# Kernel optimization log

Measured on AMD Instinct MI355X. Metric: run time of the kernel, lower is better.

Reference implementation:

```python
import jax, jax.numpy as jnp
import numpy as np

N_E = 1024
E_DIM = 256
BETA = 0.25
N = 131072


def setup_inputs() -> dict:
    key = jax.random.key(0)
    k1, k2 = jax.random.split(key)
    z = jax.random.normal(k1, (N, E_DIM), dtype=jnp.float32)
    # original init: uniform(-1/n_e, 1/n_e)
    emb_weight = jax.random.uniform(k2, (N_E, E_DIM), dtype=jnp.float32,
                                    minval=-1.0 / N_E, maxval=1.0 / N_E)
    return {"z": z, "emb_weight": emb_weight}


def reference(z, emb_weight):
    # pairwise squared distances: ||z||^2 + ||e||^2 - 2 z @ e^T   -> [N, n_e]
    d = (jnp.sum(z * z, axis=1, keepdims=True)
         + jnp.sum(emb_weight * emb_weight, axis=1)
         - 2.0 * jnp.matmul(z, emb_weight.T))
    min_encoding_indices = jnp.argmin(d, axis=1)            # [N]
    z_q = emb_weight[min_encoding_indices]                  # gather == one-hot matmul
    sg = jax.lax.stop_gradient
    loss = (jnp.mean((sg(z_q) - z) ** 2)
            + BETA * jnp.mean((z_q - sg(z)) ** 2))
    z_q_st = z + sg(z_q - z)                                # straight-through
    return z_q_st, loss, min_encoding_indices[:, None]
```

## Files before the change

### kernel.cpp

```cpp
#include <hip/hip_runtime.h>
#include <cfloat>

#define NROWS 131072
#define EDIM 256
#define NE 1024
#define DELTA 2.0e-4f

#define BM 128
#define BN 128
#define BK 32

typedef unsigned short u16;
typedef __attribute__((ext_vector_type(8))) short bf16x8;
typedef __attribute__((ext_vector_type(4))) float f32x4;

#define WS_Z2    0u
#define WS_E2    524288u
#define WS_PART  528384u
#define WS_CNT   548864u
#define WS_LIST  549120u
#define WS_CI1   1073408u
#define WS_CI2   1597696u
#define WS_FLG   2121984u
#define WS_BP    2646272u
#define WS_END   4219136u

__device__ __forceinline__ float np_sumsq256(const float* __restrict__ row) {
    float s[2];
#pragma unroll
    for (int h = 0; h < 2; ++h) {
        const float* a = row + h * 128;
        float r[8];
#pragma unroll
        for (int j = 0; j < 8; ++j) r[j] = __fmul_rn(a[j], a[j]);
        for (int i = 8; i < 128; i += 8) {
#pragma unroll
            for (int j = 0; j < 8; ++j)
                r[j] = __fadd_rn(r[j], __fmul_rn(a[i + j], a[i + j]));
        }
        s[h] = __fadd_rn(__fadd_rn(__fadd_rn(r[0], r[1]), __fadd_rn(r[2], r[3])),
                         __fadd_rn(__fadd_rn(r[4], r[5]), __fadd_rn(r[6], r[7])));
    }
    return __fadd_rn(s[0], s[1]);
}

__device__ __forceinline__ u16 bf16_rn(float x) {
    unsigned u = __float_as_uint(x);
    return (u16)((u + 0x7fffu + ((u >> 16) & 1u)) >> 16);
}

__global__ __launch_bounds__(256)
void rownorm_split_kernel(const float* __restrict__ z, float* __restrict__ z2out,
                          u16* __restrict__ zhi, u16* __restrict__ zlo) {
    __shared__ float zl[16 * 256];
    const int tid = threadIdx.x;
    const size_t base4 = (size_t)blockIdx.x * 1024;

    {
        const float4* src = reinterpret_cast<const float4*>(z) + base4;
        float4* dst = reinterpret_cast<float4*>(zl);
#pragma unroll
        for (int i = 0; i < 4; ++i) dst[tid + 256 * i] = src[tid + 256 * i];
    }
    __syncthreads();

    {
        const int row = tid >> 4;
        const int j16 = tid & 15;
        const int h = j16 >> 3, j = j16 & 7;
        const float* a = &zl[row * 256 + h * 128];
        float r = __fmul_rn(a[j], a[j]);
#pragma unroll
        for (int i = 8; i < 128; i += 8)
            r = __fadd_rn(r, __fmul_rn(a[i + j], a[i + j]));
        r = __fadd_rn(r, __shfl_xor(r, 1));
        r = __fadd_rn(r, __shfl_xor(r, 2));
        r = __fadd_rn(r, __shfl_xor(r, 4));
        r = __fadd_rn(r, __shfl_xor(r, 8));
        if (j16 == 0) z2out[blockIdx.x * 16 + row] = r;
    }

    {
        ushort4* ph = reinterpret_cast<ushort4*>(zhi) + base4;
        ushort4* pl = reinterpret_cast<ushort4*>(zlo) + base4;
        const float4* sp = reinterpret_cast<const float4*>(zl);
#pragma unroll
        for (int i = 0; i < 4; ++i) {
            const int q = tid + 256 * i;
            float4 v = sp[q];
            float xs[4] = {v.x, v.y, v.z, v.w};
            u16 hh[4], lo[4];
#pragma unroll
            for (int c = 0; c < 4; ++c) {
                u16 hv = bf16_rn(xs[c]);
                float hf = __uint_as_float(((unsigned)hv) << 16);
                hh[c] = hv;
                lo[c] = bf16_rn(__fsub_rn(xs[c], hf));
            }
            ph[q] = make_ushort4(hh[0], hh[1], hh[2], hh[3]);
            pl[q] = make_ushort4(lo[0], lo[1], lo[2], lo[3]);
        }
    }
}

__global__ __launch_bounds__(256)
void rownorm_kernel(const float* __restrict__ x, float* __restrict__ out, int nrows) {
    int row = blockIdx.x * blockDim.x + threadIdx.x;
    if (row < nrows) out[row] = np_sumsq256(x + (size_t)row * EDIM);
}

__global__ __launch_bounds__(256)
void build_b_kernel(const float* __restrict__ e, u16* __restrict__ Bp) {
    int idx = blockIdx.x * 256 + threadIdx.x;
    int row = idx >> 8, k = idx & 255;
    float x = e[idx];
    u16 hh = bf16_rn(x);
    float hf = __uint_as_float(((unsigned)hh) << 16);
    u16 lo = bf16_rn(__fsub_rn(x, hf));
    Bp[row * 512 + k] = hh;
    Bp[row * 512 + 256 + k] = lo;
}

__device__ __forceinline__ void gload_lds16(const void* g, void* lds) {
    __builtin_amdgcn_global_load_lds((const __attribute__((address_space(1))) void*)g,
                                     (__attribute__((address_space(3))) void*)lds,
                                     16, 0, 0);
}

#define LEXLT(va, ia, vb, ib) ((va) < (vb) || ((va) == (vb) && (ia) < (ib)))

#define MERGE5(a1, ai1, a2, ai2, a3, b1, bi1, b2, bi2, b3)                    \
    {                                                                         \
        float n1v, n2v, n3v; int n1i, n2i;                                    \
        if (LEXLT(a1, ai1, b1, bi1)) {                                        \
            n1v = a1; n1i = ai1;                                              \
            if (LEXLT(a2, ai2, b1, bi1)) { n2v = a2; n2i = ai2; n3v = fminf(a3, b1); } \
            else                          { n2v = b1; n2i = bi1; n3v = fminf(a2, b2); } \
        } else {                                                              \
            n1v = b1; n1i = bi1;                                              \
            if (LEXLT(b2, bi2, a1, ai1)) { n2v = b2; n2i = bi2; n3v = fminf(b3, a1); } \
            else                          { n2v = a1; n2i = ai1; n3v = fminf(b2, a2); } \
        }                                                                     \
        a1 = n1v; ai1 = n1i; a2 = n2v; ai2 = n2i; a3 = n3v;                   \
    }

__global__ __launch_bounds__(512, 2)
void vq_mfma_kernel(const u16* __restrict__ zhi, const u16* __restrict__ zlo,
                    const u16* __restrict__ Bp, const float* __restrict__ e2f,
                    int* __restrict__ ci1, int* __restrict__ ci2, int* __restrict__ cflag) {
    __shared__ __align__(16) u16  At[128 * 64];
    __shared__ __align__(16) u16  Bt[256 * 64];
    __shared__ float e2s[1024];
    __shared__ float mrg[128 * 4 * 4];

    const int tid = threadIdx.x;
    const int m0  = blockIdx.x * 128;
    const int l   = tid & 63;
    const int wid = tid >> 6;
    const int wrg = wid >> 2;
    const int wcg = wid & 3;
    const int lr  = l & 15;
    const int lg  = l >> 4;
    const int key = lr & 7;

    e2s[tid] = e2f[tid];
    e2s[tid + 512] = e2f[tid + 512];

    const int rsub = tid >> 3;
    const int lch  = (tid & 7) ^ (rsub & 7);

#define STAGE_AT(src, colc)                                                   \
    {                                                                         \
        _Pragma("unroll")                                                     \
        for (int s = 0; s < 2; ++s)                                           \
            gload_lds16((src) + (size_t)(m0 + s * 64 + rsub) * 256 + (colc) + lch * 8, \
                        At + (size_t)(s * 512 + tid) * 8);                    \
    }
#define STAGE_BT(off)                                                         \
    {                                                                         \
        _Pragma("unroll")                                                     \
        for (int s = 0; s < 4; ++s)                                           \
            gload_lds16(Bp + (size_t)(n0 + s * 64 + rsub) * 512 + (off) + lch * 8, \
                        Bt + (size_t)(s * 512 + tid) * 8);                    \
    }
#define MFMA_STEP()                                                           \
    {                                                                         \
        const u16* Ebase = Bt + (wcg * 64 + lr) * 64;                         \
        const u16* Zbase = At + (wrg * 64 + lr) * 64;                         \
        _Pragma("unroll")                                                     \
        for (int kk = 0; kk < 2; ++kk) {                                      \
            const int go = ((kk * 4 + lg) ^ key) * 8;                         \
            bf16x8 a[4], b[4];                                                \
            _Pragma("unroll")                                                 \
            for (int fr = 0; fr < 4; ++fr)                                    \
                a[fr] = *reinterpret_cast<const bf16x8*>(Ebase + fr * 1024 + go); \
            _Pragma("unroll")                                                 \
            for (int fc = 0; fc < 4; ++fc)                                    \
                b[fc] = *reinterpret_cast<const bf16x8*>(Zbase + fc * 1024 + go); \
            _Pragma("unroll")                                                 \
            for (int fr = 0; fr < 4; ++fr)                                    \
                _Pragma("unroll")                                             \
                for (int fc = 0; fc < 4; ++fc)                                \
                    acc[fr][fc] = __builtin_amdgcn_mfma_f32_16x16x32_bf16(    \
                        a[fr], b[fc], acc[fr][fc], 0, 0, 0);                  \
        }                                                                     \
    }

    float v1[4], v2[4], v3[4];
    unsigned pidx[4];
#pragma unroll
    for (int s = 0; s < 4; ++s) { v1[s] = FLT_MAX; v2[s] = FLT_MAX; v3[s] = FLT_MAX; pidx[s] = 0; }

#pragma unroll 1
    for (int nc = 0; nc < 4; ++nc) {
        const int n0 = nc * 256;
        f32x4 acc[4][4];
#pragma unroll
        for (int fr = 0; fr < 4; ++fr)
#pragma unroll
            for (int fc = 0; fc < 4; ++fc) acc[fr][fc] = (f32x4){0.f, 0.f, 0.f, 0.f};

#pragma unroll 1
        for (int j = 0; j < 4; ++j) {
            __syncthreads();
            STAGE_AT(zhi, j * 64);
            STAGE_BT(j * 64);
            asm volatile("s_waitcnt vmcnt(0)" ::: "memory");
            __syncthreads();
            MFMA_STEP();

            __syncthreads();
            STAGE_BT(256 + j * 64);
            asm volatile("s_waitcnt vmcnt(0)" ::: "memory");
            __syncthreads();
            MFMA_STEP();
        }
#pragma unroll 1
        for (int j = 0; j < 4; ++j) {
            __syncthreads();
            STAGE_AT(zlo, j * 64);
            STAGE_BT(j * 64);
            asm volatile("s_waitcnt vmcnt(0)" ::: "memory");
            __syncthreads();
            MFMA_STEP();
        }

#pragma unroll
        for (int fr = 0; fr < 4; ++fr) {
            const int cbase = n0 + wcg * 64 + fr * 16 + lg * 4;
            const float4 e2v = *reinterpret_cast<const float4*>(&e2s[cbase]);
#pragma unroll
            for (int q = 0; q < 4; ++q) {
                const unsigned n = (unsigned)(cbase + q);
                const float e2q = (q == 0) ? e2v.x : (q == 1) ? e2v.y : (q == 2) ? e2v.z : e2v.w;
#pragma unroll
                for (int fc = 0; fc < 4; ++fc) {
                    float d = __fmaf_rn(-2.0f, acc[fr][fc][q], e2q);
                    bool lt1 = d < v1[fc];
                    bool lt2 = d < v2[fc];
                    bool lt3 = d < v3[fc];
                    v3[fc] = lt2 ? v2[fc] : (lt3 ? d : v3[fc]);
                    v2[fc] = lt1 ? v1[fc] : (lt2 ? d : v2[fc]);
                    pidx[fc] = lt1 ? ((pidx[fc] << 16) | n)
                                   : (lt2 ? ((pidx[fc] & 0xffffu) | (n << 16)) : pidx[fc]);
                    v1[fc] = lt1 ? d : v1[fc];
                }
            }
        }
    }

#pragma unroll
    for (int s = 0; s < 4; ++s) {
        float a1 = v1[s], a2 = v2[s], a3 = v3[s];
        int ai1 = (int)(pidx[s] & 0xffffu), ai2 = (int)(pidx[s] >> 16);
#pragma unroll
        for (int m = 16; m <= 32; m <<= 1) {
            float b1 = __shfl_xor(a1, m), b2 = __shfl_xor(a2, m), b3 = __shfl_xor(a3, m);
            int bi1 = __shfl_xor(ai1, m), bi2 = __shfl_xor(ai2, m);
            MERGE5(a1, ai1, a2, ai2, a3, b1, bi1, b2, bi2, b3);
        }
        if (lg == 0) {
            int row = wrg * 64 + s * 16 + lr;
            float* p = &mrg[(row * 4 + wcg) * 4];
            p[0] = a1; p[1] = a2; p[2] = a3;
            p[3] = __uint_as_float(((unsigned)ai1 & 0xffffu) | ((unsigned)ai2 << 16));
        }
    }
    __syncthreads();

    if (tid < 128) {
        const float* p0 = &mrg[(tid * 4 + 0) * 4];
        float A1 = p0[0], A2 = p0[1], A3 = p0[2];
        unsigned pk = __float_as_uint(p0[3]);
        int I1 = (int)(pk & 0xffffu), I2 = (int)(pk >> 16);
#pragma unroll
        for (int w = 1; w < 4; ++w) {
            const float* p = &mrg[(tid * 4 + w) * 4];
            float b1 = p[0], b2 = p[1], b3 = p[2];
            unsigned q = __float_as_uint(p[3]);
            int bi1 = (int)(q & 0xffffu), bi2 = (int)(q >> 16);
            MERGE5(A1, I1, A2, I2, A3, b1, bi1, b2, bi2, b3);
        }
        ci1[m0 + tid] = I1;
        ci2[m0 + tid] = I2;
        cflag[m0 + tid] = (A3 - A1 <= DELTA) ? 1 : 0;
    }
}

__device__ __forceinline__ float exact_g(const float* __restrict__ zr,
                                         const float* __restrict__ er,
                                         float z2v, float e2v) {
    float m = 0.f;
    for (int k = 0; k < 256; k += 4) {
        float4 zv = *reinterpret_cast<const float4*>(zr + k);
        float4 ev = *reinterpret_cast<const float4*>(er + k);
        m = __fmaf_rn(zv.x, ev.x, m);
        m = __fmaf_rn(zv.y, ev.y, m);
        m = __fmaf_rn(zv.z, ev.z, m);
        m = __fmaf_rn(zv.w, ev.w, m);
    }
    return __fsub_rn(__fadd_rn(z2v, e2v), __fmul_rn(2.0f, m));
}

__global__ __launch_bounds__(256)
void vq_refine_kernel(const float* __restrict__ z, const float* __restrict__ e,
                      const float* __restrict__ z2g, const float* __restrict__ e2f,
                      const int* __restrict__ ci1, const int* __restrict__ ci2,
                      const int* __restrict__ cflag,
                      float* __restrict__ out_idx, int* __restrict__ list,
                      int* __restrict__ counter,
                      float* __restrict__ out_zq, double* __restrict__ partials) {
    __shared__ float  gbuf[128];
    __shared__ int    fIdx[64];
    __shared__ int    fFlag[64];
    __shared__ double dred[256];
    const int tid = threadIdx.x;
    const int r0  = blockIdx.x * 64;

    if (tid < 128) {
        int r = tid >> 1, which = tid & 1;
        int row = r0 + r;
        int c = which ? ci2[row] : ci1[row];
        gbuf[tid] = exact_g(z + (size_t)row * EDIM, e + (size_t)c * EDIM, z2g[row], e2f[c]);
    }
    __syncthreads();
    if (tid < 64) {
        int row = r0 + tid;
        int a = ci1[row], b = ci2[row];
        float ga = gbuf[tid * 2], gb = gbuf[tid * 2 + 1];
        int fi = (gb < ga || (gb == ga && b < a)) ? b : a;
        fIdx[tid] = fi;
        int fl = cflag[row];
        fFlag[tid] = fl;
        out_idx[row] = (float)fi;
        if (fl) { int p = atomicAdd(counter, 1); list[p] = row; }
    }
    __syncthreads();

    double lsum = 0.0;
    for (int r = 0; r < 64; ++r) {
        if (!fFlag[r]) {
            int row = r0 + r;
            float zv = z[(size_t)row * EDIM + tid];
            float ev = e[(size_t)fIdx[r] * EDIM + tid];
            float dd = __fsub_rn(ev, zv);
            out_zq[(size_t)row * EDIM + tid] = __fadd_rn(zv, dd);
            lsum += (double)dd * (double)dd;
        }
    }
    dred[tid] = lsum;
    __syncthreads();
#pragma unroll
    for (int s = 128; s > 0; s >>= 1) {
        if (tid < s) dred[tid] += dred[tid + s];
        __syncthreads();
    }
    if (tid == 0) partials[blockIdx.x] = dred[0];
}

__global__ __launch_bounds__(256)
void vq_fallback_kernel(const float* __restrict__ z, const float* __restrict__ e,
                        const float* __restrict__ z2g, const float* __restrict__ e2f,
                        const int* __restrict__ list, const int* __restrict__ counter,
                        float* __restrict__ out_idx, float* __restrict__ out_zq,
                        double* __restrict__ partials2) {
    __shared__ float  elds[64 * 257];
    __shared__ float  zlds[4][256];
    __shared__ float  z2s[4];
    __shared__ double dred[256];
    const int n   = *counter;
    const int tid = threadIdx.x;
    const int w   = tid >> 6;
    const int lane = tid & 63;
    double lsum = 0.0;

    for (int base = blockIdx.x * 4; base < n; base += gridDim.x * 4) {
        const int nr = min(4, n - base);
        __syncthreads();
        for (int i = tid; i < nr * 256; i += 256)
            zlds[i >> 8][i & 255] = z[(size_t)list[base + (i >> 8)] * EDIM + (i & 255)];
        if (tid < nr) z2s[tid] = z2g[list[base + tid]];

        float bv = FLT_MAX; int bi = 0x7fffffff;
        const int srow  = ((tid >> 4) & 3);
        const int scolq = (tid & 15) | ((tid >> 6) << 4);
        for (int c0 = 0; c0 < NE; c0 += 64) {
            __syncthreads();
#pragma unroll
            for (int s = 0; s < 16; ++s) {
                int row = 4 * s + srow;
                float4 v = *reinterpret_cast<const float4*>(e + (size_t)(c0 + row) * EDIM + scolq * 4);
                float* d = &elds[row * 257 + scolq * 4];
                d[0] = v.x; d[1] = v.y; d[2] = v.z; d[3] = v.w;
            }
            __syncthreads();
            const int code = c0 + lane;
            const float* er = &elds[lane * 257];
            const float* zr = zlds[w];
            float m = 0.f;
#pragma unroll 8
            for (int k = 0; k < 256; ++k)
                m = __fmaf_rn(zr[k], er[k], m);
            float g = __fsub_rn(__fadd_rn(z2s[w], e2f[code]), __fmul_rn(2.0f, m));
            if (g < bv || (g == bv && code < bi)) { bv = g; bi = code; }
        }
#pragma unroll
        for (int m2 = 1; m2 < 64; m2 <<= 1) {
            float ov = __shfl_xor(bv, m2); int oi = __shfl_xor(bi, m2);
            if (ov < bv || (ov == bv && oi < bi)) { bv = ov; bi = oi; }
        }
        if (w < nr) {
            int row = list[base + w];
            if (lane == 0) out_idx[row] = (float)bi;
            const float* er2 = e + (size_t)bi * EDIM;
            for (int c = lane; c < 256; c += 64) {
                float zv = zlds[w][c];
                float dd = __fsub_rn(er2[c], zv);
                out_zq[(size_t)row * EDIM + c] = __fadd_rn(zv, dd);
                lsum += (double)dd * (double)dd;
            }
        }
    }
    dred[tid] = lsum;
    __syncthreads();
#pragma unroll
    for (int s = 128; s > 0; s >>= 1) {
        if (tid < s) dred[tid] += dred[tid + s];
        __syncthreads();
    }
    if (tid == 0) partials2[blockIdx.x] = dred[0];
}

__global__ void vq_loss_kernel(const double* __restrict__ partials, int count,
                               float* __restrict__ out_loss) {
    __shared__ double s[256];
    const int tid = threadIdx.x;
    double v = 0.0;
    for (int i = tid; i < count; i += 256) v += partials[i];
    s[tid] = v;
    __syncthreads();
    for (int k = 128; k > 0; k >>= 1) {
        if (tid < k) s[tid] += s[tid + k];
        __syncthreads();
    }
    if (tid == 0) {
        double mean = s[0] / ((double)NROWS * (double)EDIM);
        out_loss[0] = (float)(1.25 * mean);
    }
}

__global__ __launch_bounds__(256, 2)
void vq_main_r3(const float* __restrict__ z, const float* __restrict__ e,
                const float* __restrict__ z2g, const float* __restrict__ e2g,
                float* __restrict__ out_zq, float* __restrict__ out_idx,
                double* __restrict__ partials) {
    __shared__ float A[BK][BM];
    __shared__ float Bm[BK][BN];
    __shared__ float e2s[BN];
    __shared__ int   fIdx[BM];
    __shared__ double dred[256];
    const int tid = threadIdx.x;
    const int m0 = blockIdx.x * BM;
    const int trow = tid >> 4, tcol = tid & 15;
    float z2r[8];
#pragma unroll
    for (int i = 0; i < 8; ++i) z2r[i] = z2g[m0 + trow * 8 + i];
    float bestV[8]; int bestI[8];
#pragma unroll
    for (int i = 0; i < 8; ++i) { bestV[i] = FLT_MAX; bestI[i] = 0; }
    for (int n0 = 0; n0 < NE; n0 += BN) {
        float acc[8][8];
#pragma unroll
        for (int i = 0; i < 8; ++i)
#pragma unroll
            for (int j = 0; j < 8; ++j) acc[i][j] = 0.f;
        __syncthreads();
        if (tid < BN) e2s[tid] = e2g[n0 + tid];
        for (int k0 = 0; k0 < EDIM; k0 += BK) {
            __syncthreads();
#pragma unroll
            for (int s = 0; s < 4; ++s) {
                int q = tid + 256 * s, row = q >> 3, kc = (q & 7) << 2;
                float4 va = *reinterpret_cast<const float4*>(z + (size_t)(m0 + row) * EDIM + k0 + kc);
                A[kc + 0][row] = va.x; A[kc + 1][row] = va.y; A[kc + 2][row] = va.z; A[kc + 3][row] = va.w;
                float4 vb = *reinterpret_cast<const float4*>(e + (size_t)(n0 + row) * EDIM + k0 + kc);
                Bm[kc + 0][row] = vb.x; Bm[kc + 1][row] = vb.y; Bm[kc + 2][row] = vb.z; Bm[kc + 3][row] = vb.w;
            }
            __syncthreads();
#pragma unroll
            for (int k = 0; k < BK; ++k) {
                float a[8], b[8];
                *reinterpret_cast<float4*>(&a[0]) = *reinterpret_cast<const float4*>(&A[k][trow * 8]);
                *reinterpret_cast<float4*>(&a[4]) = *reinterpret_cast<const float4*>(&A[k][trow * 8 + 4]);
                *reinterpret_cast<float4*>(&b[0]) = *reinterpret_cast<const float4*>(&Bm[k][tcol * 8]);
                *reinterpret_cast<float4*>(&b[4]) = *reinterpret_cast<const float4*>(&Bm[k][tcol * 8 + 4]);
#pragma unroll
                for (int i = 0; i < 8; ++i)
#pragma unroll
                    for (int j = 0; j < 8; ++j) acc[i][j] = __fmaf_rn(a[i], b[j], acc[i][j]);
            }
        }
#pragma unroll
        for (int i = 0; i < 8; ++i)
#pragma unroll
            for (int j = 0; j < 8; ++j) {
                int n = n0 + tcol * 8 + j;
                float d = __fsub_rn(__fadd_rn(z2r[i], e2s[tcol * 8 + j]), __fmul_rn(2.0f, acc[i][j]));
                if (d < bestV[i]) { bestV[i] = d; bestI[i] = n; }
            }
    }
    __syncthreads();
    float* red_v = &A[0][0];
    int* red_i = reinterpret_cast<int*>(&Bm[0][0]);
#pragma unroll
    for (int i = 0; i < 8; ++i) {
        int row = trow * 8 + i;
        red_v[row * 16 + tcol] = bestV[i];
        red_i[row * 16 + tcol] = bestI[i];
    }
    __syncthreads();
    if (tid < BM) {
        float b1 = FLT_MAX; int i1 = 0x7fffffff;
        for (int t = 0; t < 16; ++t) {
            float v = red_v[tid * 16 + t]; int id = red_i[tid * 16 + t];
            if (v < b1 || (v == b1 && id < i1)) { b1 = v; i1 = id; }
        }
        fIdx[tid] = i1;
        out_idx[m0 + tid] = (float)i1;
    }
    __syncthreads();
    double lsum = 0.0;
    for (int r = 0; r < BM; ++r) {
        int fi = fIdx[r];
        float zv = z[(size_t)(m0 + r) * EDIM + tid];
        float ev = e[(size_t)fi * EDIM + tid];
        float dd = __fsub_rn(ev, zv);
        out_zq[(size_t)(m0 + r) * EDIM + tid] = __fadd_rn(zv, dd);
        lsum += (double)dd * (double)dd;
    }
    dred[tid] = lsum;
    __syncthreads();
#pragma unroll
    for (int s = 128; s > 0; s >>= 1) {
        if (tid < s) dred[tid] += dred[tid + s];
        __syncthreads();
    }
    if (tid == 0) partials[blockIdx.x] = dred[0];
}

extern "C" void kernel_launch(void* const* d_in, const int* in_sizes, int n_in,
                              void* d_out, int out_size, void* d_ws, size_t ws_size,
                              hipStream_t stream) {
    (void)n_in; (void)out_size;
    const float* z = (const float*)d_in[0];
    const float* e = (const float*)d_in[1];
    if (in_sizes[0] == NE * EDIM) { const float* t = z; z = e; e = t; }
    float* out      = (float*)d_out;
    float* out_zq   = out;
    float* out_loss = out + (size_t)NROWS * EDIM;
    float* out_idx  = out_loss + 1;

    char* ws = (char*)d_ws;
    float*  z2g      = (float*)(ws + WS_Z2);
    float*  e2f      = (float*)(ws + WS_E2);
    double* partials = (double*)(ws + WS_PART);

    rownorm_kernel<<<(NE + 255) / 256, 256, 0, stream>>>(e, e2f, NE);

    if (ws_size >= WS_END) {
        int* cnt  = (int*)(ws + WS_CNT);
        int* list = (int*)(ws + WS_LIST);
        int* ci1  = (int*)(ws + WS_CI1);
        int* ci2  = (int*)(ws + WS_CI2);
        int* flg  = (int*)(ws + WS_FLG);
        u16* Bp   = (u16*)(ws + WS_BP);
        u16* zhi  = (u16*)d_out;
        u16* zlo  = zhi + (size_t)NROWS * EDIM;

        hipMemsetAsync(cnt, 0, 4, stream);
        rownorm_split_kernel<<<NROWS / 16, 256, 0, stream>>>(z, z2g, zhi, zlo);
        build_b_kernel<<<NE * EDIM / 256, 256, 0, stream>>>(e, Bp);
        vq_mfma_kernel<<<NROWS / 128, 512, 0, stream>>>(zhi, zlo, Bp, e2f, ci1, ci2, flg);
        vq_refine_kernel<<<NROWS / 64, 256, 0, stream>>>(z, e, z2g, e2f, ci1, ci2, flg,
                                                         out_idx, list, cnt, out_zq, partials);
        vq_fallback_kernel<<<512, 256, 0, stream>>>(z, e, z2g, e2f, list, cnt,
                                                    out_idx, out_zq, partials + 2048);
        vq_loss_kernel<<<1, 256, 0, stream>>>(partials, 2560, out_loss);
    } else {
        rownorm_kernel<<<NROWS / 256, 256, 0, stream>>>(z, z2g, NROWS);
        vq_main_r3<<<NROWS / BM, 256, 0, stream>>>(z, e, z2g, e2f, out_zq, out_idx, partials);
        vq_loss_kernel<<<1, 256, 0, stream>>>(partials, 1024, out_loss);
    }
}
```

Baseline: 592.0 us.

## Double-buffer LDS tiles and enlarge MFMA block tile to 256 rows

Doubles the row tile per block from 128 to 256 and reorganizes waves as 4x2, with each wave computing an 8x4 fragment grid. It also double-buffers the A and B LDS tiles and unrolls the K schedule into explicit prefetch stages, using partial vmcnt waits so global-to-LDS loads overlap MFMA work. The goal is more data reuse per tile and hiding load latency instead of waiting for all loads before each step. In exchange, LDS use rises to about 128KB per block and the accumulators double, which can cut occupancy or force register spills under launch_bounds(512,2).

```diff
diff --git a/kernel.cpp b/kernel.cpp
--- a/kernel.cpp
+++ b/kernel.cpp
@@ -144,21 +144,24 @@
         a1 = n1v; ai1 = n1i; a2 = n2v; ai2 = n2i; a3 = n3v;                   \
     }
 
+#define WAITVM(N) asm volatile("s_waitcnt vmcnt(" #N ")" ::: "memory")
+#define RBAR()    asm volatile("s_barrier" ::: "memory")
+
 __global__ __launch_bounds__(512, 2)
 void vq_mfma_kernel(const u16* __restrict__ zhi, const u16* __restrict__ zlo,
                     const u16* __restrict__ Bp, const float* __restrict__ e2f,
                     int* __restrict__ ci1, int* __restrict__ ci2, int* __restrict__ cflag) {
-    __shared__ __align__(16) u16  At[128 * 64];
-    __shared__ __align__(16) u16  Bt[256 * 64];
+    __shared__ __align__(16) u16  At[2][256 * 64];
+    __shared__ __align__(16) u16  Bt[2][256 * 64];
     __shared__ float e2s[1024];
-    __shared__ float mrg[128 * 4 * 4];
+    __shared__ float mrg[256 * 2 * 4];
 
     const int tid = threadIdx.x;
-    const int m0  = blockIdx.x * 128;
+    const int m0  = blockIdx.x * 256;
     const int l   = tid & 63;
     const int wid = tid >> 6;
-    const int wrg = wid >> 2;
-    const int wcg = wid & 3;
+    const int wrg = wid >> 1;
+    const int wcg = wid & 1;
     const int lr  = l & 15;
     const int lg  = l >> 4;
     const int key = lr & 7;
@@ -169,36 +172,36 @@
     const int rsub = tid >> 3;
     const int lch  = (tid & 7) ^ (rsub & 7);
 
-#define STAGE_AT(src, colc)                                                   \
-    {                                                                         \
-        _Pragma("unroll")                                                     \
-        for (int s = 0; s < 2; ++s)                                           \
-            gload_lds16((src) + (size_t)(m0 + s * 64 + rsub) * 256 + (colc) + lch * 8, \
-                        At + (size_t)(s * 512 + tid) * 8);                    \
-    }
-#define STAGE_BT(off)                                                         \
+#define SAT(BUF, SRC, COLC)                                                   \
     {                                                                         \
         _Pragma("unroll")                                                     \
         for (int s = 0; s < 4; ++s)                                           \
-            gload_lds16(Bp + (size_t)(n0 + s * 64 + rsub) * 512 + (off) + lch * 8, \
-                        Bt + (size_t)(s * 512 + tid) * 8);                    \
-    }
-#define MFMA_STEP()                                                           \
+            gload_lds16((SRC) + (size_t)(m0 + s * 64 + rsub) * 256 + (COLC) + lch * 8, \
+                        At[BUF] + (size_t)(s * 512 + tid) * 8);               \
+    }
+#define SBT(BUF, NB, OFF)                                                     \
     {                                                                         \
-        const u16* Ebase = Bt + (wcg * 64 + lr) * 64;                         \
-        const u16* Zbase = At + (wrg * 64 + lr) * 64;                         \
+        _Pragma("unroll")                                                     \
+        for (int s = 0; s < 4; ++s)                                           \
+            gload_lds16(Bp + (size_t)((NB) + s * 64 + rsub) * 512 + (OFF) + lch * 8, \
+                        Bt[BUF] + (size_t)(s * 512 + tid) * 8);               \
+    }
+#define MSTEP(RA, RB)                                                         \
+    {                                                                         \
+        const u16* Eb = Bt[RB] + (wcg * 128 + lr) * 64;                       \
+        const u16* Zb = At[RA] + (wrg * 64 + lr) * 64;                        \
         _Pragma("unroll")                                                     \
         for (int kk = 0; kk < 2; ++kk) {                                      \
             const int go = ((kk * 4 + lg) ^ key) * 8;                         \
-            bf16x8 a[4], b[4];                                                \
+            bf16x8 a[8], b[4];                                                \
             _Pragma("unroll")                                                 \
-            for (int fr = 0; fr < 4; ++fr)                                    \
-                a[fr] = *reinterpret_cast<const bf16x8*>(Ebase + fr * 1024 + go); \
+            for (int fr = 0; fr < 8; ++fr)                                    \
+                a[fr] = *reinterpret_cast<const bf16x8*>(Eb + fr * 1024 + go);\
             _Pragma("unroll")                                                 \
             for (int fc = 0; fc < 4; ++fc)                                    \
-                b[fc] = *reinterpret_cast<const bf16x8*>(Zbase + fc * 1024 + go); \
+                b[fc] = *reinterpret_cast<const bf16x8*>(Zb + fc * 1024 + go);\
             _Pragma("unroll")                                                 \
-            for (int fr = 0; fr < 4; ++fr)                                    \
+            for (int fr = 0; fr < 8; ++fr)                                    \
                 _Pragma("unroll")                                             \
                 for (int fc = 0; fc < 4; ++fc)                                \
                     acc[fr][fc] = __builtin_amdgcn_mfma_f32_16x16x32_bf16(    \
@@ -211,43 +214,39 @@
 #pragma unroll
     for (int s = 0; s < 4; ++s) { v1[s] = FLT_MAX; v2[s] = FLT_MAX; v3[s] = FLT_MAX; pidx[s] = 0; }
 
+    f32x4 acc[8][4];
+
+    SAT(0, zhi, 0);
+    SBT(0, 0, 0);
+    WAITVM(0);
+    RBAR();
+
 #pragma unroll 1
     for (int nc = 0; nc < 4; ++nc) {
         const int n0 = nc * 256;
-        f32x4 acc[4][4];
-#pragma unroll
-        for (int fr = 0; fr < 4; ++fr)
+#pragma unroll
+        for (int fr = 0; fr < 8; ++fr)
 #pragma unroll
             for (int fc = 0; fc < 4; ++fc) acc[fr][fc] = (f32x4){0.f, 0.f, 0.f, 0.f};
 
-#pragma unroll 1
-        for (int j = 0; j < 4; ++j) {
-            __syncthreads();
-            STAGE_AT(zhi, j * 64);
-            STAGE_BT(j * 64);
-            asm volatile("s_waitcnt vmcnt(0)" ::: "memory");
-            __syncthreads();
-            MFMA_STEP();
-
-            __syncthreads();
-            STAGE_BT(256 + j * 64);
-            asm volatile("s_waitcnt vmcnt(0)" ::: "memory");
-            __syncthreads();
-            MFMA_STEP();
-        }
-#pragma unroll 1
-        for (int j = 0; j < 4; ++j) {
-            __syncthreads();
-            STAGE_AT(zlo, j * 64);
-            STAGE_BT(j * 64);
-            asm volatile("s_waitcnt vmcnt(0)" ::: "memory");
-            __syncthreads();
-            MFMA_STEP();
-        }
-
-#pragma unroll
-        for (int fr = 0; fr < 4; ++fr) {
-            const int cbase = n0 + wcg * 64 + fr * 16 + lg * 4;
+         SBT(1, n0, 256);                      WAITVM(4); RBAR(); MSTEP(0, 0); RBAR();
+         SAT(1, zhi, 64);  SBT(0, n0, 64);     WAITVM(8); RBAR(); MSTEP(0, 1); RBAR();
+         SBT(1, n0, 320);                      WAITVM(4); RBAR(); MSTEP(1, 0); RBAR();
+         SAT(0, zhi, 128); SBT(0, n0, 128);    WAITVM(8); RBAR(); MSTEP(1, 1); RBAR();
+         SBT(1, n0, 384);                      WAITVM(4); RBAR(); MSTEP(0, 0); RBAR();
+         SAT(1, zhi, 192); SBT(0, n0, 192);    WAITVM(8); RBAR(); MSTEP(0, 1); RBAR();
+         SBT(1, n0, 448);                      WAITVM(4); RBAR(); MSTEP(1, 0); RBAR();
+         SAT(0, zlo, 0);   SBT(0, n0, 0);      WAITVM(8); RBAR(); MSTEP(1, 1); RBAR();
+         SAT(1, zlo, 64);  SBT(1, n0, 64);     WAITVM(8); RBAR(); MSTEP(0, 0); RBAR();
+         SAT(0, zlo, 128); SBT(0, n0, 128);    WAITVM(8); RBAR(); MSTEP(1, 1); RBAR();
+         SAT(1, zlo, 192); SBT(1, n0, 192);    WAITVM(8); RBAR(); MSTEP(0, 0); RBAR();
+        if (nc < 3) { SAT(0, zhi, 0); SBT(0, n0 + 256, 0); WAITVM(8); }
+        else        { WAITVM(0); }
+        RBAR(); MSTEP(1, 1); RBAR();
+
+#pragma unroll
+        for (int fr = 0; fr < 8; ++fr) {
+            const int cbase = n0 + wcg * 128 + fr * 16 + lg * 4;
             const float4 e2v = *reinterpret_cast<const float4*>(&e2s[cbase]);
 #pragma unroll
             for (int q = 0; q < 4; ++q) {
@@ -281,26 +280,23 @@
         }
         if (lg == 0) {
             int row = wrg * 64 + s * 16 + lr;
-            float* p = &mrg[(row * 4 + wcg) * 4];
+            float* p = &mrg[(row * 2 + wcg) * 4];
             p[0] = a1; p[1] = a2; p[2] = a3;
             p[3] = __uint_as_float(((unsigned)ai1 & 0xffffu) | ((unsigned)ai2 << 16));
         }
     }
     __syncthreads();
 
-    if (tid < 128) {
-        const float* p0 = &mrg[(tid * 4 + 0) * 4];
+    if (tid < 256) {
+        const float* p0 = &mrg[(tid * 2 + 0) * 4];
         float A1 = p0[0], A2 = p0[1], A3 = p0[2];
         unsigned pk = __float_as_uint(p0[3]);
         int I1 = (int)(pk & 0xffffu), I2 = (int)(pk >> 16);
-#pragma unroll
-        for (int w = 1; w < 4; ++w) {
-            const float* p = &mrg[(tid * 4 + w) * 4];
-            float b1 = p[0], b2 = p[1], b3 = p[2];
-            unsigned q = __float_as_uint(p[3]);
-            int bi1 = (int)(q & 0xffffu), bi2 = (int)(q >> 16);
-            MERGE5(A1, I1, A2, I2, A3, b1, bi1, b2, bi2, b3);
-        }
+        const float* p = &mrg[(tid * 2 + 1) * 4];
+        float b1 = p[0], b2 = p[1], b3 = p[2];
+        unsigned q = __float_as_uint(p[3]);
+        int bi1 = (int)(q & 0xffffu), bi2 = (int)(q >> 16);
+        MERGE5(A1, I1, A2, I2, A3, b1, bi1, b2, bi2, b3);
         ci1[m0 + tid] = I1;
         ci2[m0 + tid] = I2;
         cflag[m0 + tid] = (A3 - A1 <= DELTA) ? 1 : 0;
@@ -600,7 +596,7 @@
         hipMemsetAsync(cnt, 0, 4, stream);
         rownorm_split_kernel<<<NROWS / 16, 256, 0, stream>>>(z, z2g, zhi, zlo);
         build_b_kernel<<<NE * EDIM / 256, 256, 0, stream>>>(e, Bp);
-        vq_mfma_kernel<<<NROWS / 128, 512, 0, stream>>>(zhi, zlo, Bp, e2f, ci1, ci2, flg);
+        vq_mfma_kernel<<<NROWS / 256, 512, 0, stream>>>(zhi, zlo, Bp, e2f, ci1, ci2, flg);
         vq_refine_kernel<<<NROWS / 64, 256, 0, stream>>>(z, e, z2g, e2f, ci1, ci2, flg,
                                                          out_idx, list, cnt, out_zq, partials);
         vq_fallback_kernel<<<512, 256, 0, stream>>>(z, e, z2g, e2f, list, cnt,
```

New measurement: 675.7 us. 14.1% more time.
